# Performance work log

Hardware: AMD Instinct MI355X
Metric: run time of the kernel (lower is better)

The kernel has to match this reference:

```python
import jax, jax.numpy as jnp
import numpy as np

N = 100_000   # nodes
E = 1_280_000 # edges
F_IN = 64
HID = 64

def setup_inputs() -> dict:
    key = jax.random.key(0)
    ks = jax.random.split(key, 5)
    x = jax.random.normal(ks[0], (N, F_IN), dtype=jnp.float32)
    edge_index = jax.random.randint(ks[1], (2, E), 0, N, dtype=jnp.int32)
    edge_weight = jax.random.uniform(ks[2], (E,), dtype=jnp.float32)
    s1 = 1.0 / np.sqrt(F_IN)
    W1 = jax.random.uniform(ks[3], (F_IN, HID), minval=-s1, maxval=s1, dtype=jnp.float32)
    b1 = jnp.zeros((HID,), jnp.float32)
    s2 = 1.0 / np.sqrt(HID)
    W2 = jax.random.uniform(ks[4], (HID, 1), minval=-s2, maxval=s2, dtype=jnp.float32)
    b2 = jnp.zeros((1,), jnp.float32)
    return {"x": x, "edge_index": edge_index, "edge_weight": edge_weight,
            "W1": W1, "b1": b1, "W2": W2, "b2": b2}


def reference(x, edge_index, edge_weight, W1, b1, W2, b2):
    # eval mode: edge dropout and feature dropout are identity.
    # GCNConv with add_self_loops=True: A_hat = A + I, D_hat^-1/2 A_hat D_hat^-1/2.
    row, col = edge_index[0], edge_index[1]
    sl = jnp.arange(N, dtype=row.dtype)
    row = jnp.concatenate([row, sl])
    col = jnp.concatenate([col, sl])
    w = jnp.concatenate([edge_weight, jnp.ones((N,), edge_weight.dtype)])
    # symmetric normalization (shared by both conv layers)
    deg = jax.ops.segment_sum(w, col, num_segments=N)          # [N]
    dinv = jnp.where(deg > 0, jax.lax.rsqrt(deg), 0.0)
    norm = dinv[row] * w * dinv[col]                           # [E+N]

    def gcn(h):  # h: [N, d] already linearly transformed
        msg = h[row] * norm[:, None]                           # gather + scale
        return jax.ops.segment_sum(msg, col, num_segments=N)   # scatter-add

    h = gcn(x @ W1) + b1          # conv1
    h = jax.nn.relu(h)            # relu (dropout = identity in eval)
    out = gcn(h @ W2) + b2        # conv2 -> [N, 1]
    return out
```

## Files before the change

kernel.cpp:

```cpp
#include <hip/hip_runtime.h>
#include <hip/hip_fp16.h>

#define CNT_SHIFT 26
#define DEG_MASK  ((1u << CNT_SHIFT) - 1)
#define DEG_SCALE 1048576.0f
#define CAP 8192
#define GSTRIDE 16

typedef __attribute__((ext_vector_type(8))) short short8;
typedef __attribute__((ext_vector_type(4))) float v4f;

__device__ __forceinline__ unsigned short f_to_h16(float f) {
    return __half_as_ushort(__float2half(f));
}
__device__ __forceinline__ float h16_to_f(unsigned short u) {
    return __half2float(__ushort_as_half(u));
}
__device__ __forceinline__ unsigned short f_to_bf16(float f) {
    unsigned int u = __float_as_uint(f);
    u += 0x7fffu + ((u >> 16) & 1u);
    return (unsigned short)(u >> 16);
}
__device__ __forceinline__ unsigned long long mkrec(int r, int c, float wv) {
    return (unsigned long long)r | ((unsigned long long)(c & 511) << 17)
         | ((unsigned long long)f_to_h16(wv) << 26);
}

__global__ __launch_bounds__(256) void k_scatter_gemm(
        const int4* __restrict__ row4, const int4* __restrict__ col4, const float4* __restrict__ w4,
        const int* __restrict__ row, const int* __restrict__ col, const float* __restrict__ w,
        unsigned* __restrict__ gcur, unsigned long long* __restrict__ binrec,
        const float* __restrict__ x, const float* __restrict__ W1,
        char* __restrict__ h1q, float* __restrict__ scales,
        int E4, int rem, int nBlkE, int nGemm, int n, int nbkt) {
    __shared__ int h[256];
    int blk = blockIdx.x, t = threadIdx.x;
    if (blk < nBlkE) {
        h[t] = 0;
        __syncthreads();
        int base = blk * 1024;
#pragma unroll
        for (int k = 0; k < 4; ++k) {
            int g = base + k * 256 + t;
            if (g < E4) {
                int4 c = col4[g];
                atomicAdd(&h[c.x >> 9], 1);
                atomicAdd(&h[c.y >> 9], 1);
                atomicAdd(&h[c.z >> 9], 1);
                atomicAdd(&h[c.w >> 9], 1);
            }
        }
        if (blk == 0 && t < rem) atomicAdd(&h[col[4 * E4 + t] >> 9], 1);
        __syncthreads();
        if (t < nbkt) {
            int bb = t + (blk % nbkt);
            bb -= (bb >= nbkt) ? nbkt : 0;
            int cnt = h[bb];
            int runbase = 0;
            if (cnt > 0) runbase = (int)atomicAdd(&gcur[(size_t)bb * GSTRIDE], (unsigned)cnt);
            h[bb] = bb * CAP + runbase;
        }
        __syncthreads();
#pragma unroll
        for (int k = 0; k < 4; ++k) {
            int g = base + k * 256 + t;
            if (g < E4) {
                int4   r = row4[g];
                int4   c = col4[g];
                float4 v = w4[g];
                { int pos = atomicAdd(&h[c.x >> 9], 1); binrec[pos] = mkrec(r.x, c.x, v.x); }
                { int pos = atomicAdd(&h[c.y >> 9], 1); binrec[pos] = mkrec(r.y, c.y, v.y); }
                { int pos = atomicAdd(&h[c.z >> 9], 1); binrec[pos] = mkrec(r.z, c.z, v.z); }
                { int pos = atomicAdd(&h[c.w >> 9], 1); binrec[pos] = mkrec(r.w, c.w, v.w); }
            }
        }
        if (blk == 0 && t < rem) {
            int e = 4 * E4 + t;
            int c = col[e];
            int pos = atomicAdd(&h[c >> 9], 1);
            binrec[pos] = mkrec(row[e], c, w[e]);
        }
    } else {
        int b = blk - nBlkE;
        int lane = t & 63;
        int wave = t >> 6;
        int q   = lane >> 4;
        int n16 = lane & 15;
        short8 bf[8];
#pragma unroll
        for (int ct = 0; ct < 4; ++ct) {
#pragma unroll
            for (int hh = 0; hh < 2; ++hh) {
                short8 v;
#pragma unroll
                for (int j = 0; j < 8; ++j)
                    v[j] = (short)f_to_bf16(W1[(hh * 32 + q * 8 + j) * 64 + ct * 16 + n16]);
                bf[ct * 2 + hh] = v;
            }
        }
        int ntile = (n + 15) >> 4;
        int stride = nGemm * 4;
        for (int tile = b * 4 + wave; tile < ntile; tile += stride) {
            int base = tile << 4;
            short8 a0, a1;
            if (base + 16 <= n) {
                const float* xr = x + (size_t)(base + n16) * 64 + q * 8;
                float4 u0 = *(const float4*)(xr);
                float4 u1 = *(const float4*)(xr + 4);
                float4 u2 = *(const float4*)(xr + 32);
                float4 u3 = *(const float4*)(xr + 36);
                a0[0] = (short)f_to_bf16(u0.x); a0[1] = (short)f_to_bf16(u0.y);
                a0[2] = (short)f_to_bf16(u0.z); a0[3] = (short)f_to_bf16(u0.w);
                a0[4] = (short)f_to_bf16(u1.x); a0[5] = (short)f_to_bf16(u1.y);
                a0[6] = (short)f_to_bf16(u1.z); a0[7] = (short)f_to_bf16(u1.w);
                a1[0] = (short)f_to_bf16(u2.x); a1[1] = (short)f_to_bf16(u2.y);
                a1[2] = (short)f_to_bf16(u2.z); a1[3] = (short)f_to_bf16(u2.w);
                a1[4] = (short)f_to_bf16(u3.x); a1[5] = (short)f_to_bf16(u3.y);
                a1[6] = (short)f_to_bf16(u3.z); a1[7] = (short)f_to_bf16(u3.w);
            } else {
                bool ok = (base + n16) < n;
                const float* xr = x + (size_t)(ok ? (base + n16) : 0) * 64 + q * 8;
#pragma unroll
                for (int j = 0; j < 8; ++j) {
                    a0[j] = ok ? (short)f_to_bf16(xr[j])      : (short)0;
                    a1[j] = ok ? (short)f_to_bf16(xr[32 + j]) : (short)0;
                }
            }
            v4f acc0 = {0.f, 0.f, 0.f, 0.f}, acc1 = acc0, acc2 = acc0, acc3 = acc0;
            acc0 = __builtin_amdgcn_mfma_f32_16x16x32_bf16(a0, bf[0], acc0, 0, 0, 0);
            acc0 = __builtin_amdgcn_mfma_f32_16x16x32_bf16(a1, bf[1], acc0, 0, 0, 0);
            acc1 = __builtin_amdgcn_mfma_f32_16x16x32_bf16(a0, bf[2], acc1, 0, 0, 0);
            acc1 = __builtin_amdgcn_mfma_f32_16x16x32_bf16(a1, bf[3], acc1, 0, 0, 0);
            acc2 = __builtin_amdgcn_mfma_f32_16x16x32_bf16(a0, bf[4], acc2, 0, 0, 0);
            acc2 = __builtin_amdgcn_mfma_f32_16x16x32_bf16(a1, bf[5], acc2, 0, 0, 0);
            acc3 = __builtin_amdgcn_mfma_f32_16x16x32_bf16(a0, bf[6], acc3, 0, 0, 0);
            acc3 = __builtin_amdgcn_mfma_f32_16x16x32_bf16(a1, bf[7], acc3, 0, 0, 0);
#pragma unroll
            for (int r = 0; r < 4; ++r) {
                int rowg = base + q * 4 + r;
                if (rowg >= n) break;
                float m = fmaxf(fmaxf(fabsf(acc0[r]), fabsf(acc1[r])),
                                fmaxf(fabsf(acc2[r]), fabsf(acc3[r])));
                m = fmaxf(m, __shfl_xor(m, 1, 64));
                m = fmaxf(m, __shfl_xor(m, 2, 64));
                m = fmaxf(m, __shfl_xor(m, 4, 64));
                m = fmaxf(m, __shfl_xor(m, 8, 64));
                m = fmaxf(m, 1e-20f);
                float inv = 127.0f / m;
                unsigned char* dst = (unsigned char*)h1q + (size_t)rowg * 64 + n16;
                dst[0]  = (unsigned char)(__float2int_rn(acc0[r] * inv) + 128);
                dst[16] = (unsigned char)(__float2int_rn(acc1[r] * inv) + 128);
                dst[32] = (unsigned char)(__float2int_rn(acc2[r] * inv) + 128);
                dst[48] = (unsigned char)(__float2int_rn(acc3[r] * inv) + 128);
                if (n16 == 0) scales[rowg] = m * (1.0f / 127.0f);
            }
        }
    }
}

__global__ __launch_bounds__(256) void k_bucket(
        const unsigned long long* __restrict__ binrec, const unsigned* __restrict__ gcur,
        float* __restrict__ dinv, int* __restrict__ off, int* __restrict__ bktend,
        unsigned* __restrict__ ep, float* __restrict__ scales,
        int N, int nbkt) {
    __shared__ unsigned cnt[512];
    __shared__ int   loff[512];
    __shared__ int   ssum[256];
    int b = blockIdx.x, t = threadIdx.x;
    int e0 = b * CAP;
    int tot = (int)gcur[(size_t)b * GSTRIDE];
    int e1 = e0 + tot;
    cnt[t] = 0u; cnt[t + 256] = 0u;
    __syncthreads();
    unsigned epw[32];
    unsigned crk[32];
#pragma unroll
    for (int k = 0; k < 32; ++k) {
        int i = e0 + t + k * 256;
        if (i < e1) {
            unsigned long long rec = binrec[i];
            int cl = (int)((rec >> 17) & 511);
            unsigned hb = (unsigned)((rec >> 26) & 0xFFFF);
            float wv = h16_to_f((unsigned short)hb);
            unsigned old = atomicAdd(&cnt[cl],
                                     (1u << CNT_SHIFT) + (unsigned)(wv * DEG_SCALE + 0.5f));
            unsigned rank = old >> CNT_SHIFT;
            epw[k] = ((unsigned)(rec & 0x1FFFF) << 15) | (hb & 0x7fffu);
            crk[k] = ((unsigned)cl << 16) | rank;
        }
    }
    __syncthreads();
    unsigned p0 = cnt[2 * t], p1 = cnt[2 * t + 1];
    int c0 = (int)(p0 >> CNT_SHIFT), c1 = (int)(p1 >> CNT_SHIFT);
    float d0 = rsqrtf((float)(p0 & DEG_MASK) * (1.0f / DEG_SCALE) + 1.0f);
    float d1 = rsqrtf((float)(p1 & DEG_MASK) * (1.0f / DEG_SCALE) + 1.0f);
    int ps = c0 + c1;
    ssum[t] = ps;
    __syncthreads();
    for (int o = 1; o < 256; o <<= 1) {
        int v = (t >= o) ? ssum[t - o] : 0;
        __syncthreads();
        ssum[t] += v;
        __syncthreads();
    }
    int excl = ssum[t] - ps;
    loff[2 * t] = excl;
    loff[2 * t + 1] = excl + c0;
    int id0 = (b << 9) + 2 * t, id1 = id0 + 1;
    if (id0 < N) { dinv[id0] = d0; scales[id0] *= d0; off[id0] = e0 + excl; }
    if (id1 < N) { dinv[id1] = d1; scales[id1] *= d1; off[id1] = e0 + excl + c0; }
    if (t == 0) bktend[b] = e1;
    __syncthreads();
#pragma unroll
    for (int k = 0; k < 32; ++k) {
        int i = e0 + t + k * 256;
        if (i < e1) {
            int cl   = (int)(crk[k] >> 16);
            int rank = (int)(crk[k] & 0xFFFFu);
            ep[e0 + loff[cl] + rank] = epw[k];
        }
    }
}

__global__ __launch_bounds__(256) void k_agg1(
        const char* __restrict__ h1q_, const float* __restrict__ scales,
        const int* __restrict__ off, const int* __restrict__ bktend,
        const unsigned* __restrict__ ep,
        const float* __restrict__ dinv, const float* __restrict__ b1,
        const float* __restrict__ W2,
        float* __restrict__ h2, int n) {
    const unsigned char* __restrict__ h1q = (const unsigned char*)h1q_;
    __shared__ uint2 tbl[4][4][65];
    int t = threadIdx.x;
    int lane = t & 63, wave = t >> 6, grp = lane >> 4, f15 = lane & 15, fl = f15 * 4;
    int i = blockIdx.x * 16 + wave * 4 + grp;
    bool alive = i < n;
    int s = 0, s1 = 0;
    if (alive) {
        s = off[i];
        s1 = (((i & 511) == 511) || (i == n - 1)) ? bktend[i >> 9] : off[i + 1];
    }
    int deg = s1 - s;
    int md = max(deg, __shfl_xor(deg, 16, 64));
    md = max(md, __shfl_xor(md, 32, 64));
    float di = alive ? dinv[i] : 0.f;
    float4 acc = {0.f, 0.f, 0.f, 0.f};
    float S = 0.f;
    if (alive) {
        unsigned q4 = *(const unsigned*)(h1q + ((size_t)i << 6) + fl);
        float si = scales[i];
        acc.x = (float)(q4 & 0xffu)         * si;
        acc.y = (float)((q4 >> 8) & 0xffu)  * si;
        acc.z = (float)((q4 >> 16) & 0xffu) * si;
        acc.w = (float)(q4 >> 24)           * si;
        S = si;
    }
    for (int c0 = 0; c0 < md; c0 += 64) {
        int remg = deg - c0;
        int mrem = md - c0; if (mrem > 64) mrem = 64;
        for (int k = 0; k * 16 < mrem; ++k) {
            int slot = k * 16 + f15;
            unsigned src = 0u; float m = 0.f;
            if (slot < remg) {
                unsigned e = ep[s + c0 + slot];
                src = e >> 15;
                m = scales[src] * h16_to_f((unsigned short)(e & 0x7fffu));
            }
            tbl[wave][grp][slot] = make_uint2(src, __float_as_uint(m));
        }
        for (int j = 0; j < mrem; j += 4) {
            uint2 t0 = tbl[wave][grp][j];
            uint2 t1 = tbl[wave][grp][j + 1];
            uint2 t2 = tbl[wave][grp][j + 2];
            uint2 t3 = tbl[wave][grp][j + 3];
            unsigned q0 = *(const unsigned*)(h1q + ((size_t)t0.x << 6) + fl);
            unsigned q1 = *(const unsigned*)(h1q + ((size_t)t1.x << 6) + fl);
            unsigned q2 = *(const unsigned*)(h1q + ((size_t)t2.x << 6) + fl);
            unsigned q3 = *(const unsigned*)(h1q + ((size_t)t3.x << 6) + fl);
            float m0 = __uint_as_float(t0.y), m1 = __uint_as_float(t1.y);
            float m2 = __uint_as_float(t2.y), m3 = __uint_as_float(t3.y);
            acc.x = fmaf((float)(q0 & 0xffu),         m0, acc.x);
            acc.y = fmaf((float)((q0 >> 8) & 0xffu),  m0, acc.y);
            acc.z = fmaf((float)((q0 >> 16) & 0xffu), m0, acc.z);
            acc.w = fmaf((float)(q0 >> 24),           m0, acc.w);
            acc.x = fmaf((float)(q1 & 0xffu),         m1, acc.x);
            acc.y = fmaf((float)((q1 >> 8) & 0xffu),  m1, acc.y);
            acc.z = fmaf((float)((q1 >> 16) & 0xffu), m1, acc.z);
            acc.w = fmaf((float)(q1 >> 24),           m1, acc.w);
            acc.x = fmaf((float)(q2 & 0xffu),         m2, acc.x);
            acc.y = fmaf((float)((q2 >> 8) & 0xffu),  m2, acc.y);
            acc.z = fmaf((float)((q2 >> 16) & 0xffu), m2, acc.z);
            acc.w = fmaf((float)(q2 >> 24),           m2, acc.w);
            acc.x = fmaf((float)(q3 & 0xffu),         m3, acc.x);
            acc.y = fmaf((float)((q3 >> 8) & 0xffu),  m3, acc.y);
            acc.z = fmaf((float)((q3 >> 16) & 0xffu), m3, acc.z);
            acc.w = fmaf((float)(q3 >> 24),           m3, acc.w);
            S += (m0 + m1) + (m2 + m3);
        }
    }
    acc.x = fmaf(S, -128.f, acc.x);
    acc.y = fmaf(S, -128.f, acc.y);
    acc.z = fmaf(S, -128.f, acc.z);
    acc.w = fmaf(S, -128.f, acc.w);
    float4 bb = *(const float4*)(b1 + fl);
    float4 ww = *(const float4*)(W2 + fl);
    float p = fmaxf(fmaf(di, acc.x, bb.x), 0.f) * ww.x
            + fmaxf(fmaf(di, acc.y, bb.y), 0.f) * ww.y
            + fmaxf(fmaf(di, acc.z, bb.z), 0.f) * ww.z
            + fmaxf(fmaf(di, acc.w, bb.w), 0.f) * ww.w;
#pragma unroll
    for (int o = 1; o < 16; o <<= 1) p += __shfl_xor(p, o, 64);
    if (f15 == 0 && alive) h2[i] = di * p;
}

__global__ void k_agg2(const float* __restrict__ h2,
                       const int* __restrict__ off, const int* __restrict__ bktend,
                       const unsigned* __restrict__ ep, const float* __restrict__ dinv,
                       const float* __restrict__ b2, float* __restrict__ out, int n) {
    int i = blockIdx.x * 256 + threadIdx.x;
    if (i >= n) return;
    float acc = h2[i];
    int s = off[i];
    int s1 = (((i & 511) == 511) || (i == n - 1)) ? bktend[i >> 9] : off[i + 1];
    for (; s + 8 <= s1; s += 8) {
        unsigned e0 = ep[s],     e1 = ep[s + 1], e2 = ep[s + 2], e3 = ep[s + 3];
        unsigned e4 = ep[s + 4], e5 = ep[s + 5], e6 = ep[s + 6], e7 = ep[s + 7];
        float v0 = h2[e0 >> 15], v1 = h2[e1 >> 15], v2 = h2[e2 >> 15], v3 = h2[e3 >> 15];
        float v4 = h2[e4 >> 15], v5 = h2[e5 >> 15], v6 = h2[e6 >> 15], v7 = h2[e7 >> 15];
        acc = fmaf(v0, h16_to_f((unsigned short)(e0 & 0x7fff)), acc);
        acc = fmaf(v1, h16_to_f((unsigned short)(e1 & 0x7fff)), acc);
        acc = fmaf(v2, h16_to_f((unsigned short)(e2 & 0x7fff)), acc);
        acc = fmaf(v3, h16_to_f((unsigned short)(e3 & 0x7fff)), acc);
        acc = fmaf(v4, h16_to_f((unsigned short)(e4 & 0x7fff)), acc);
        acc = fmaf(v5, h16_to_f((unsigned short)(e5 & 0x7fff)), acc);
        acc = fmaf(v6, h16_to_f((unsigned short)(e6 & 0x7fff)), acc);
        acc = fmaf(v7, h16_to_f((unsigned short)(e7 & 0x7fff)), acc);
    }
    for (; s + 4 <= s1; s += 4) {
        unsigned e0 = ep[s], e1 = ep[s + 1], e2 = ep[s + 2], e3 = ep[s + 3];
        float v0 = h2[e0 >> 15], v1 = h2[e1 >> 15], v2 = h2[e2 >> 15], v3 = h2[e3 >> 15];
        acc = fmaf(v0, h16_to_f((unsigned short)(e0 & 0x7fff)), acc);
        acc = fmaf(v1, h16_to_f((unsigned short)(e1 & 0x7fff)), acc);
        acc = fmaf(v2, h16_to_f((unsigned short)(e2 & 0x7fff)), acc);
        acc = fmaf(v3, h16_to_f((unsigned short)(e3 & 0x7fff)), acc);
    }
    for (; s < s1; ++s) {
        unsigned e = ep[s];
        acc = fmaf(h2[e >> 15], h16_to_f((unsigned short)(e & 0x7fff)), acc);
    }
    out[i] = dinv[i] * acc + b2[0];
}

extern "C" void kernel_launch(void* const* d_in, const int* in_sizes, int n_in,
                              void* d_out, int out_size, void* d_ws, size_t ws_size,
                              hipStream_t stream) {
    const float* x  = (const float*)d_in[0];
    const int*   ei = (const int*)d_in[1];
    const float* w  = (const float*)d_in[2];
    const float* W1 = (const float*)d_in[3];
    const float* b1 = (const float*)d_in[4];
    const float* W2 = (const float*)d_in[5];
    const float* b2 = (const float*)d_in[6];
    float* out = (float*)d_out;

    const int N = in_sizes[0] / 64;
    const int E = in_sizes[2];
    const int* row = ei;
    const int* col = ei + E;

    const int nbkt  = (N + 511) >> 9;
    const int E4    = E / 4;
    const int rem   = E - 4 * E4;
    const int nBlkE = (E4 + 1023) / 1024;
    const int nGemm = 1024;

    char* p = (char*)d_ws;
    auto take = [&](size_t bytes) { char* q = p; p += (bytes + 15) & ~(size_t)15; return q; };
    unsigned long long* binrec = (unsigned long long*)take((size_t)nbkt * CAP * 8);
    unsigned* gcur = (unsigned*)take((size_t)nbkt * GSTRIDE * 4);
    int* bktend  = (int*)take((size_t)nbkt * 4);
    char* h1q    = (char*)take((size_t)N * 64);
    float* scales= (float*)take((size_t)N * 4);
    float* dinv  = (float*)take((size_t)N * 4);
    int*   off   = (int*)take((size_t)(N + 1) * 4);
    unsigned* ep = (unsigned*)take((size_t)nbkt * CAP * 4);
    float* h2    = (float*)take((size_t)N * 4);

    (void)hipMemsetAsync(gcur, 0, (size_t)nbkt * GSTRIDE * 4, stream);
    k_scatter_gemm<<<nBlkE + nGemm, 256, 0, stream>>>(
        (const int4*)row, (const int4*)col, (const float4*)w,
        row, col, w, gcur, binrec, x, W1, h1q, scales,
        E4, rem, nBlkE, nGemm, N, nbkt);
    k_bucket<<<nbkt, 256, 0, stream>>>(binrec, gcur, dinv, off, bktend, ep, scales, N, nbkt);
    k_agg1<<<(N + 15) / 16, 256, 0, stream>>>(h1q, scales, off, bktend, ep, dinv, b1, W2, h2, N);
    k_agg2<<<(N + 255) / 256, 256, 0, stream>>>(h2, off, bktend, ep, dinv, b2, out, N);
}
```

Measured before the change: 161.6 us.

## Shrink column buckets to 128-node slabs and simplify per-bucket scan

Changes the edge binning from 512-node buckets (CAP 8192) to 128-node slabs (CAP 2048), giving about 782 buckets instead of 196. The bucket kernel then has more blocks with less work each, uses fewer registers, and replaces the 256-wide shared-memory scan with a wave shuffle scan. The scatter kernel reuses the column values it already loaded instead of reading them again. The costs are more global atomic slots per scatter block, a larger shared histogram, and a lower per-bucket capacity, which could overflow on skewed degree distributions.

```diff
diff --git a/kernel.cpp b/kernel.cpp
--- a/kernel.cpp
+++ b/kernel.cpp
@@ -4,7 +4,9 @@
 #define CNT_SHIFT 26
 #define DEG_MASK  ((1u << CNT_SHIFT) - 1)
 #define DEG_SCALE 1048576.0f
-#define CAP 8192
+#define SLAB_LOG 7
+#define SLAB 128
+#define CAP 2048
 #define GSTRIDE 16
 
 typedef __attribute__((ext_vector_type(8))) short short8;
@@ -22,8 +24,8 @@
     return (unsigned short)(u >> 16);
 }
 __device__ __forceinline__ unsigned long long mkrec(int r, int c, float wv) {
-    return (unsigned long long)r | ((unsigned long long)(c & 511) << 17)
-         | ((unsigned long long)f_to_h16(wv) << 26);
+    return (unsigned long long)r | ((unsigned long long)(c & (SLAB - 1)) << 17)
+         | ((unsigned long long)f_to_h16(wv) << 24);
 }
 
 __global__ __launch_bounds__(256) void k_scatter_gemm(
@@ -33,28 +35,30 @@
         const float* __restrict__ x, const float* __restrict__ W1,
         char* __restrict__ h1q, float* __restrict__ scales,
         int E4, int rem, int nBlkE, int nGemm, int n, int nbkt) {
-    __shared__ int h[256];
+    __shared__ int h[1024];
     int blk = blockIdx.x, t = threadIdx.x;
     if (blk < nBlkE) {
-        h[t] = 0;
+        for (int idx = t; idx < nbkt; idx += 256) h[idx] = 0;
         __syncthreads();
         int base = blk * 1024;
+        int4 cs[4];
 #pragma unroll
         for (int k = 0; k < 4; ++k) {
             int g = base + k * 256 + t;
             if (g < E4) {
                 int4 c = col4[g];
-                atomicAdd(&h[c.x >> 9], 1);
-                atomicAdd(&h[c.y >> 9], 1);
-                atomicAdd(&h[c.z >> 9], 1);
-                atomicAdd(&h[c.w >> 9], 1);
-            }
-        }
-        if (blk == 0 && t < rem) atomicAdd(&h[col[4 * E4 + t] >> 9], 1);
+                cs[k] = c;
+                atomicAdd(&h[c.x >> SLAB_LOG], 1);
+                atomicAdd(&h[c.y >> SLAB_LOG], 1);
+                atomicAdd(&h[c.z >> SLAB_LOG], 1);
+                atomicAdd(&h[c.w >> SLAB_LOG], 1);
+            }
+        }
+        if (blk == 0 && t < rem) atomicAdd(&h[col[4 * E4 + t] >> SLAB_LOG], 1);
         __syncthreads();
-        if (t < nbkt) {
-            int bb = t + (blk % nbkt);
-            bb -= (bb >= nbkt) ? nbkt : 0;
+        for (int idx = t; idx < nbkt; idx += 256) {
+            int bb = idx + blk;
+            while (bb >= nbkt) bb -= nbkt;
             int cnt = h[bb];
             int runbase = 0;
             if (cnt > 0) runbase = (int)atomicAdd(&gcur[(size_t)bb * GSTRIDE], (unsigned)cnt);
@@ -66,18 +70,18 @@
             int g = base + k * 256 + t;
             if (g < E4) {
                 int4   r = row4[g];
-                int4   c = col4[g];
+                int4   c = cs[k];
                 float4 v = w4[g];
-                { int pos = atomicAdd(&h[c.x >> 9], 1); binrec[pos] = mkrec(r.x, c.x, v.x); }
-                { int pos = atomicAdd(&h[c.y >> 9], 1); binrec[pos] = mkrec(r.y, c.y, v.y); }
-                { int pos = atomicAdd(&h[c.z >> 9], 1); binrec[pos] = mkrec(r.z, c.z, v.z); }
-                { int pos = atomicAdd(&h[c.w >> 9], 1); binrec[pos] = mkrec(r.w, c.w, v.w); }
+                { int pos = atomicAdd(&h[c.x >> SLAB_LOG], 1); binrec[pos] = mkrec(r.x, c.x, v.x); }
+                { int pos = atomicAdd(&h[c.y >> SLAB_LOG], 1); binrec[pos] = mkrec(r.y, c.y, v.y); }
+                { int pos = atomicAdd(&h[c.z >> SLAB_LOG], 1); binrec[pos] = mkrec(r.z, c.z, v.z); }
+                { int pos = atomicAdd(&h[c.w >> SLAB_LOG], 1); binrec[pos] = mkrec(r.w, c.w, v.w); }
             }
         }
         if (blk == 0 && t < rem) {
             int e = 4 * E4 + t;
             int c = col[e];
-            int pos = atomicAdd(&h[c >> 9], 1);
+            int pos = atomicAdd(&h[c >> SLAB_LOG], 1);
             binrec[pos] = mkrec(row[e], c, w[e]);
         }
     } else {
@@ -163,24 +167,25 @@
         float* __restrict__ dinv, int* __restrict__ off, int* __restrict__ bktend,
         unsigned* __restrict__ ep, float* __restrict__ scales,
         int N, int nbkt) {
-    __shared__ unsigned cnt[512];
-    __shared__ int   loff[512];
-    __shared__ int   ssum[256];
+    __shared__ unsigned cnt[SLAB];
+    __shared__ int   loff[SLAB];
+    __shared__ int   wtot;
     int b = blockIdx.x, t = threadIdx.x;
+    int lane = t & 63;
     int e0 = b * CAP;
     int tot = (int)gcur[(size_t)b * GSTRIDE];
     int e1 = e0 + tot;
-    cnt[t] = 0u; cnt[t + 256] = 0u;
+    if (t < SLAB) cnt[t] = 0u;
     __syncthreads();
-    unsigned epw[32];
-    unsigned crk[32];
-#pragma unroll
-    for (int k = 0; k < 32; ++k) {
+    unsigned epw[8];
+    unsigned crk[8];
+#pragma unroll
+    for (int k = 0; k < 8; ++k) {
         int i = e0 + t + k * 256;
         if (i < e1) {
             unsigned long long rec = binrec[i];
-            int cl = (int)((rec >> 17) & 511);
-            unsigned hb = (unsigned)((rec >> 26) & 0xFFFF);
+            int cl = (int)((rec >> 17) & (SLAB - 1));
+            unsigned hb = (unsigned)((rec >> 24) & 0xFFFF);
             float wv = h16_to_f((unsigned short)hb);
             unsigned old = atomicAdd(&cnt[cl],
                                      (1u << CNT_SHIFT) + (unsigned)(wv * DEG_SCALE + 0.5f));
@@ -190,29 +195,33 @@
         }
     }
     __syncthreads();
-    unsigned p0 = cnt[2 * t], p1 = cnt[2 * t + 1];
-    int c0 = (int)(p0 >> CNT_SHIFT), c1 = (int)(p1 >> CNT_SHIFT);
-    float d0 = rsqrtf((float)(p0 & DEG_MASK) * (1.0f / DEG_SCALE) + 1.0f);
-    float d1 = rsqrtf((float)(p1 & DEG_MASK) * (1.0f / DEG_SCALE) + 1.0f);
-    int ps = c0 + c1;
-    ssum[t] = ps;
+    unsigned pk = 0u;
+    int c = 0;
+    if (t < SLAB) { pk = cnt[t]; c = (int)(pk >> CNT_SHIFT); }
+    int incl = c;
+#pragma unroll
+    for (int o = 1; o < 64; o <<= 1) {
+        int v = __shfl_up(incl, o, 64);
+        if (lane >= o) incl += v;
+    }
+    if (t == 63) wtot = incl;
     __syncthreads();
-    for (int o = 1; o < 256; o <<= 1) {
-        int v = (t >= o) ? ssum[t - o] : 0;
-        __syncthreads();
-        ssum[t] += v;
-        __syncthreads();
-    }
-    int excl = ssum[t] - ps;
-    loff[2 * t] = excl;
-    loff[2 * t + 1] = excl + c0;
-    int id0 = (b << 9) + 2 * t, id1 = id0 + 1;
-    if (id0 < N) { dinv[id0] = d0; scales[id0] *= d0; off[id0] = e0 + excl; }
-    if (id1 < N) { dinv[id1] = d1; scales[id1] *= d1; off[id1] = e0 + excl + c0; }
+    if (t >= 64 && t < SLAB) incl += wtot;
+    if (t < SLAB) {
+        int excl = incl - c;
+        loff[t] = excl;
+        int id = (b << SLAB_LOG) + t;
+        if (id < N) {
+            float d = rsqrtf((float)(pk & DEG_MASK) * (1.0f / DEG_SCALE) + 1.0f);
+            dinv[id] = d;
+            scales[id] *= d;
+            off[id] = e0 + excl;
+        }
+    }
     if (t == 0) bktend[b] = e1;
     __syncthreads();
 #pragma unroll
-    for (int k = 0; k < 32; ++k) {
+    for (int k = 0; k < 8; ++k) {
         int i = e0 + t + k * 256;
         if (i < e1) {
             int cl   = (int)(crk[k] >> 16);
@@ -238,7 +247,7 @@
     int s = 0, s1 = 0;
     if (alive) {
         s = off[i];
-        s1 = (((i & 511) == 511) || (i == n - 1)) ? bktend[i >> 9] : off[i + 1];
+        s1 = (((i & (SLAB - 1)) == (SLAB - 1)) || (i == n - 1)) ? bktend[i >> SLAB_LOG] : off[i + 1];
     }
     int deg = s1 - s;
     int md = max(deg, __shfl_xor(deg, 16, 64));
@@ -321,7 +330,7 @@
     if (i >= n) return;
     float acc = h2[i];
     int s = off[i];
-    int s1 = (((i & 511) == 511) || (i == n - 1)) ? bktend[i >> 9] : off[i + 1];
+    int s1 = (((i & (SLAB - 1)) == (SLAB - 1)) || (i == n - 1)) ? bktend[i >> SLAB_LOG] : off[i + 1];
     for (; s + 8 <= s1; s += 8) {
         unsigned e0 = ep[s],     e1 = ep[s + 1], e2 = ep[s + 2], e3 = ep[s + 3];
         unsigned e4 = ep[s + 4], e5 = ep[s + 5], e6 = ep[s + 6], e7 = ep[s + 7];
@@ -368,7 +377,7 @@
     const int* row = ei;
     const int* col = ei + E;
 
-    const int nbkt  = (N + 511) >> 9;
+    const int nbkt  = (N + SLAB - 1) >> SLAB_LOG;
     const int E4    = E / 4;
     const int rem   = E - 4 * E4;
     const int nBlkE = (E4 + 1023) / 1024;
```

After: 161.9 us. No clear change (+0.2%).
